# Kernel tuning notes

Measured on AMD Instinct MI355X. Metric: run time of the kernel, lower is better.

## Reference

```python
import jax, jax.numpy as jnp
import numpy as np

EPS = 1e-7


def _chamfer(p1, p2):
    # p1: (bs, N, 3), p2: (bs, M, 3)
    n1 = jnp.sum(p1 * p1, axis=-1)                    # (bs, N)
    n2 = jnp.sum(p2 * p2, axis=-1)                    # (bs, M)
    inner = jnp.einsum('bnd,bmd->bnm', p1, p2)        # (bs, N, M)
    d2 = n1[:, :, None] + n2[:, None, :] - 2.0 * inner
    d = jnp.sqrt(jnp.maximum(d2, 1e-12))              # L2 norm, as torch.norm(dim=3)
    # symmetric chamfer: sum of per-point nearest-neighbor distances, both ways
    cd = jnp.sum(jnp.min(d, axis=2)) + jnp.sum(jnp.min(d, axis=1))
    return cd


def setup_inputs() -> dict:
    key = jax.random.key(0)
    k1, k2, k3, k4, k5, k6, k7 = jax.random.split(key, 7)
    bs, K, N, M = 8, 1000, 4096, 4096
    return {
        'prob_pred': jax.random.uniform(k1, (bs, K), dtype=jnp.float32),
        'prob_target': jax.random.uniform(k2, (bs, K), dtype=jnp.float32),
        'x_diff_pred': jax.random.normal(k3, (bs, N, 3), dtype=jnp.float32),
        'x_diff_target': jax.random.normal(k4, (bs, M, 3), dtype=jnp.float32),
        'mu': jax.random.normal(k5, (K,), dtype=jnp.float32),
        'lower_bound': jax.random.uniform(k6, (K,), dtype=jnp.float32),
        'upper_bound': jax.random.uniform(k7, (K,), dtype=jnp.float32),
    }


def reference(prob_pred, prob_target, x_diff_pred, x_diff_target, mu, lower_bound, upper_bound):
    K = upper_bound.shape[0]
    # box-constraint term
    cr = jnp.abs(mu.reshape(lower_bound.shape)) - (lower_bound + upper_bound) / 2.0 + 1.0 / K
    CR = jnp.sum(jax.nn.relu(cr))
    # BCE with mean reduction (clamp like torch's internal log clamping)
    p = jnp.clip(prob_pred, EPS, 1.0 - EPS)
    BCE = -jnp.mean(prob_target * jnp.log(p) + (1.0 - prob_target) * jnp.log1p(-p))
    # chamfer distance
    CD = _chamfer(x_diff_pred, x_diff_target)
    return BCE + CD + CR
```

## Files before the change

### kernel.cpp

```cpp
#include <hip/hip_runtime.h>
#include <math.h>

#define EPSF 1e-7f
#define NP 4096

typedef __attribute__((ext_vector_type(8)))  short  short8;
typedef __attribute__((ext_vector_type(8)))  __bf16 bf16x8;
typedef __attribute__((ext_vector_type(16))) float  f32x16;

__device__ __forceinline__ unsigned short bf16_rn(float x) {
    unsigned int u = __float_as_uint(x);
    unsigned int r = u + 0x7FFFu + ((u >> 16) & 1u);
    return (unsigned short)(r >> 16);
}
__device__ __forceinline__ float bf16_to_f(unsigned short h) {
    return __uint_as_float(((unsigned int)h) << 16);
}

__device__ __forceinline__ void fold16(const f32x16& d, float& ra, float& rb) {
    ra = fminf(fminf(d[0],  d[1]),  ra);
    rb = fminf(fminf(d[2],  d[3]),  rb);
    ra = fminf(fminf(d[4],  d[5]),  ra);
    rb = fminf(fminf(d[6],  d[7]),  rb);
    ra = fminf(fminf(d[8],  d[9]),  ra);
    rb = fminf(fminf(d[10], d[11]), rb);
    ra = fminf(fminf(d[12], d[13]), ra);
    rb = fminf(fminf(d[14], d[15]), rb);
}

__device__ __forceinline__ bf16x8 make_qfrag(float x, float y, float z, int kg) {
    float m2x = -2.f * x, m2y = -2.f * y, m2z = -2.f * z;
    unsigned short xh = bf16_rn(m2x), yh = bf16_rn(m2y), zh = bf16_rn(m2z);
    unsigned short xl = bf16_rn(m2x - bf16_to_f(xh));
    unsigned short yl = bf16_rn(m2y - bf16_to_f(yh));
    unsigned short zl = bf16_rn(m2z - bf16_to_f(zh));
    short8 s;
    if (kg == 0)
        s = short8{(short)xh,(short)yh,(short)zh,(short)xl,(short)yl,(short)zl,(short)xh,(short)yh};
    else
        s = short8{(short)zh,(short)0x3F80,(short)0x3F80,0,0,0,0,0};
    return __builtin_bit_cast(bf16x8, s);
}

__global__ __launch_bounds__(256, 2) void chamfer_all(
    const float* __restrict__ pred, const float* __restrict__ targ,
    float* __restrict__ parts)
{
    const int tid  = threadIdx.x;
    const int lane = tid & 63, w = tid >> 6, kg = lane >> 5;
    const int strip = blockIdx.x;
    const int combo = blockIdx.y;
    const int dir = combo >> 3, b = combo & 7;

    __shared__ char  lds[65536];
    __shared__ float red[4];

    const float* Q = (dir ? targ : pred) + (size_t)b * NP * 3;
    const int q = strip * 128 + w * 32 + (lane & 31);
    const float qx = Q[q * 3], qy = Q[q * 3 + 1], qz = Q[q * 3 + 2];
    const bf16x8 frag = make_qfrag(qx, qy, qz, kg);
    const float n1 = fmaf(qx, qx, fmaf(qy, qy, qz * qz));

    const float* D = (dir ? pred : targ) + (size_t)b * NP * 3;

    float r0 = 3.4e38f, r1 = 3.4e38f;
    const f32x16 zero = {0.f};

    for (int half = 0; half < 2; ++half) {
#pragma unroll
        for (int i = 0; i < 8; ++i) {
            const int pl = tid + i * 256;
            const float* dp = D + (size_t)(half * 2048 + pl) * 3;
            float x = dp[0], y = dp[1], z = dp[2];
            float n2 = fmaf(x, x, fmaf(y, y, z * z));
            unsigned short xh = bf16_rn(x), yh = bf16_rn(y), zh = bf16_rn(z);
            unsigned short xl = bf16_rn(x - bf16_to_f(xh));
            unsigned short yl = bf16_rn(y - bf16_to_f(yh));
            unsigned short zl = bf16_rn(z - bf16_to_f(zh));
            unsigned short nh = bf16_rn(n2);
            unsigned short nl = bf16_rn(n2 - bf16_to_f(nh));
            short8 k0 = short8{(short)xh,(short)yh,(short)zh,
                               (short)xh,(short)yh,(short)zh,
                               (short)xl,(short)yl};
            short8 k1 = short8{(short)zl,(short)nh,(short)nl,0,0,0,0,0};
            char* base = lds + (pl >> 5) * 1024 + (pl & 31) * 16;
            *(short8*)base         = k0;
            *(short8*)(base + 512) = k1;
        }
        __syncthreads();

#pragma unroll 4
        for (int t = 0; t < 64; ++t) {
            bf16x8 af = *(const bf16x8*)(lds + t * 1024 + kg * 512 + (lane & 31) * 16);
            f32x16 d = __builtin_amdgcn_mfma_f32_32x32x16_bf16(af, frag, zero, 0, 0, 0);
            fold16(d, r0, r1);
        }
        __syncthreads();
    }

    float r = fminf(r0, r1);
    r = fminf(r, __shfl_xor(r, 32));
    float dist = sqrtf(fmaxf(r + n1, 1e-12f));
    for (int off = 16; off; off >>= 1) dist += __shfl_xor(dist, off);
    if (lane == 0) red[w] = dist;
    __syncthreads();
    if (tid == 0)
        parts[blockIdx.y * 32 + blockIdx.x] = red[0] + red[1] + red[2] + red[3];
}

__global__ __launch_bounds__(256) void finalize_kernel(
    const float* __restrict__ parts,
    const float* __restrict__ prob_pred, const float* __restrict__ prob_target,
    const float* __restrict__ mu, const float* __restrict__ lb,
    const float* __restrict__ ub,
    float* __restrict__ out, int nprob, int K)
{
    const int tid = threadIdx.x;

    float bce = 0.f;
    const float pmax = 1.0f - EPSF;
    for (int i = tid; i < nprob; i += 256) {
        float p = prob_pred[i];
        p = fminf(fmaxf(p, EPSF), pmax);
        float t = prob_target[i];
        bce += t * logf(p) + (1.0f - t) * log1pf(-p);
    }

    float cr = 0.f;
    const float invK = 1.0f / (float)K;
    for (int i = tid; i < K; i += 256) {
        float c = fabsf(mu[i]) - 0.5f * (lb[i] + ub[i]) + invK;
        cr += fmaxf(c, 0.f);
    }

    float v1 = parts[tid] + parts[tid + 256] + cr;
    float v2 = bce;
    for (int off = 32; off; off >>= 1) {
        v1 += __shfl_xor(v1, off);
        v2 += __shfl_xor(v2, off);
    }
    __shared__ float s1[4], s2[4];
    if ((tid & 63) == 0) { s1[tid >> 6] = v1; s2[tid >> 6] = v2; }
    __syncthreads();
    if (tid == 0) {
        float V1 = s1[0] + s1[1] + s1[2] + s1[3];
        float V2 = s2[0] + s2[1] + s2[2] + s2[3];
        out[0] = V1 - V2 / (float)nprob;
    }
}

extern "C" void kernel_launch(void* const* d_in, const int* in_sizes, int n_in,
                              void* d_out, int out_size, void* d_ws, size_t ws_size,
                              hipStream_t stream) {
    const float* prob_pred   = (const float*)d_in[0];
    const float* prob_target = (const float*)d_in[1];
    const float* x_pred      = (const float*)d_in[2];
    const float* x_target    = (const float*)d_in[3];
    const float* mu          = (const float*)d_in[4];
    const float* lb          = (const float*)d_in[5];
    const float* ub          = (const float*)d_in[6];
    float* out   = (float*)d_out;
    float* parts = (float*)d_ws;

    const int K     = in_sizes[4];
    const int nprob = in_sizes[0];

    dim3 grid(32, 16);
    chamfer_all<<<grid, 256, 0, stream>>>(x_pred, x_target, parts);
    finalize_kernel<<<1, 256, 0, stream>>>(parts, prob_pred, prob_target,
                                           mu, lb, ub, out, nprob, K);
}
```

Measured before the change: 29.70 us.

## Stage full reference panel once, split across 8 waves, two query tiles each

The chamfer kernel now loads and packs all 4096 reference points into a 128 KB LDS panel in one pass. Each 512-thread block handles 256 queries, with two query fragments per wave so each LDS A-fragment feeds two MFMAs. The two wave halves each scan half of the panel and merge their minima through LDS. The next fragment load is software-prefetched. The grid halves to 256 blocks, which cuts redundant reference loading and packing, but the large LDS footprint limits occupancy to one block per CU.

```diff
diff --git a/kernel.cpp b/kernel.cpp
--- a/kernel.cpp
+++ b/kernel.cpp
@@ -42,70 +42,91 @@
     return __builtin_bit_cast(bf16x8, s);
 }
 
-__global__ __launch_bounds__(256, 2) void chamfer_all(
+__global__ __launch_bounds__(512, 2) void chamfer_fused(
     const float* __restrict__ pred, const float* __restrict__ targ,
     float* __restrict__ parts)
 {
     const int tid  = threadIdx.x;
     const int lane = tid & 63, w = tid >> 6, kg = lane >> 5;
+    const int half = w >> 2;
     const int strip = blockIdx.x;
     const int combo = blockIdx.y;
     const int dir = combo >> 3, b = combo & 7;
 
-    __shared__ char  lds[65536];
-    __shared__ float red[4];
+    __shared__ char  panel[131072];
+    __shared__ float redbuf[512];
+    __shared__ float red4[4];
 
     const float* Q = (dir ? targ : pred) + (size_t)b * NP * 3;
-    const int q = strip * 128 + w * 32 + (lane & 31);
-    const float qx = Q[q * 3], qy = Q[q * 3 + 1], qz = Q[q * 3 + 2];
-    const bf16x8 frag = make_qfrag(qx, qy, qz, kg);
-    const float n1 = fmaf(qx, qx, fmaf(qy, qy, qz * qz));
+    const int qA = strip * 256 + (w & 3) * 64 + (lane & 31);
+    const int qB = qA + 32;
+    const float ax = Q[qA * 3], ay = Q[qA * 3 + 1], az = Q[qA * 3 + 2];
+    const float bx = Q[qB * 3], by = Q[qB * 3 + 1], bz = Q[qB * 3 + 2];
+    const bf16x8 fragA = make_qfrag(ax, ay, az, kg);
+    const bf16x8 fragB = make_qfrag(bx, by, bz, kg);
+    const float n1A = fmaf(ax, ax, fmaf(ay, ay, az * az));
+    const float n1B = fmaf(bx, bx, fmaf(by, by, bz * bz));
 
     const float* D = (dir ? pred : targ) + (size_t)b * NP * 3;
+#pragma unroll
+    for (int i = 0; i < 8; ++i) {
+        const int pt = i * 512 + tid;
+        const float* dp = D + (size_t)pt * 3;
+        float x = dp[0], y = dp[1], z = dp[2];
+        float n2 = fmaf(x, x, fmaf(y, y, z * z));
+        unsigned short xh = bf16_rn(x), yh = bf16_rn(y), zh = bf16_rn(z);
+        unsigned short xl = bf16_rn(x - bf16_to_f(xh));
+        unsigned short yl = bf16_rn(y - bf16_to_f(yh));
+        unsigned short zl = bf16_rn(z - bf16_to_f(zh));
+        unsigned short nh = bf16_rn(n2);
+        unsigned short nl = bf16_rn(n2 - bf16_to_f(nh));
+        short8 k0 = short8{(short)xh,(short)yh,(short)zh,
+                           (short)xh,(short)yh,(short)zh,
+                           (short)xl,(short)yl};
+        short8 k1 = short8{(short)zl,(short)nh,(short)nl,0,0,0,0,0};
+        char* base = panel + (pt >> 5) * 1024 + (pt & 31) * 16;
+        *(short8*)base         = k0;
+        *(short8*)(base + 512) = k1;
+    }
+    __syncthreads();
 
-    float r0 = 3.4e38f, r1 = 3.4e38f;
+    float rA0 = 3.4e38f, rA1 = 3.4e38f, rB0 = 3.4e38f, rB1 = 3.4e38f;
     const f32x16 zero = {0.f};
+    const char* abase = panel + (size_t)half * 65536 + kg * 512 + (lane & 31) * 16;
 
-    for (int half = 0; half < 2; ++half) {
-#pragma unroll
-        for (int i = 0; i < 8; ++i) {
-            const int pl = tid + i * 256;
-            const float* dp = D + (size_t)(half * 2048 + pl) * 3;
-            float x = dp[0], y = dp[1], z = dp[2];
-            float n2 = fmaf(x, x, fmaf(y, y, z * z));
-            unsigned short xh = bf16_rn(x), yh = bf16_rn(y), zh = bf16_rn(z);
-            unsigned short xl = bf16_rn(x - bf16_to_f(xh));
-            unsigned short yl = bf16_rn(y - bf16_to_f(yh));
-            unsigned short zl = bf16_rn(z - bf16_to_f(zh));
-            unsigned short nh = bf16_rn(n2);
-            unsigned short nl = bf16_rn(n2 - bf16_to_f(nh));
-            short8 k0 = short8{(short)xh,(short)yh,(short)zh,
-                               (short)xh,(short)yh,(short)zh,
-                               (short)xl,(short)yl};
-            short8 k1 = short8{(short)zl,(short)nh,(short)nl,0,0,0,0,0};
-            char* base = lds + (pl >> 5) * 1024 + (pl & 31) * 16;
-            *(short8*)base         = k0;
-            *(short8*)(base + 512) = k1;
-        }
-        __syncthreads();
-
+    bf16x8 af = *(const bf16x8*)(abase);
 #pragma unroll 4
-        for (int t = 0; t < 64; ++t) {
-            bf16x8 af = *(const bf16x8*)(lds + t * 1024 + kg * 512 + (lane & 31) * 16);
-            f32x16 d = __builtin_amdgcn_mfma_f32_32x32x16_bf16(af, frag, zero, 0, 0, 0);
-            fold16(d, r0, r1);
-        }
-        __syncthreads();
+    for (int t = 0; t < 63; ++t) {
+        bf16x8 afn = *(const bf16x8*)(abase + (t + 1) * 1024);
+        f32x16 d0 = __builtin_amdgcn_mfma_f32_32x32x16_bf16(af, fragA, zero, 0, 0, 0);
+        f32x16 d1 = __builtin_amdgcn_mfma_f32_32x32x16_bf16(af, fragB, zero, 0, 0, 0);
+        fold16(d0, rA0, rA1);
+        fold16(d1, rB0, rB1);
+        af = afn;
+    }
+    {
+        f32x16 d0 = __builtin_amdgcn_mfma_f32_32x32x16_bf16(af, fragA, zero, 0, 0, 0);
+        f32x16 d1 = __builtin_amdgcn_mfma_f32_32x32x16_bf16(af, fragB, zero, 0, 0, 0);
+        fold16(d0, rA0, rA1);
+        fold16(d1, rB0, rB1);
     }
 
-    float r = fminf(r0, r1);
-    r = fminf(r, __shfl_xor(r, 32));
-    float dist = sqrtf(fmaxf(r + n1, 1e-12f));
-    for (int off = 16; off; off >>= 1) dist += __shfl_xor(dist, off);
-    if (lane == 0) red[w] = dist;
+    float rA = fminf(rA0, rA1);  rA = fminf(rA, __shfl_xor(rA, 32));
+    float rB = fminf(rB0, rB1);  rB = fminf(rB, __shfl_xor(rB, 32));
+    float val = (lane < 32) ? (rA + n1A) : (rB + n1B);
+    __syncthreads();
+    redbuf[half * 256 + (w & 3) * 64 + lane] = val;
+    __syncthreads();
+
+    if (tid < 256) {
+        float m = fminf(redbuf[tid], redbuf[256 + tid]);
+        float dist = sqrtf(fmaxf(m, 1e-12f));
+        for (int off = 32; off; off >>= 1) dist += __shfl_xor(dist, off);
+        if ((tid & 63) == 0) red4[tid >> 6] = dist;
+    }
     __syncthreads();
     if (tid == 0)
-        parts[blockIdx.y * 32 + blockIdx.x] = red[0] + red[1] + red[2] + red[3];
+        parts[blockIdx.y * 16 + blockIdx.x] = red4[0] + red4[1] + red4[2] + red4[3];
 }
 
 __global__ __launch_bounds__(256) void finalize_kernel(
@@ -133,7 +154,7 @@
         cr += fmaxf(c, 0.f);
     }
 
-    float v1 = parts[tid] + parts[tid + 256] + cr;
+    float v1 = parts[tid] + cr;
     float v2 = bce;
     for (int off = 32; off; off >>= 1) {
         v1 += __shfl_xor(v1, off);
@@ -165,8 +186,8 @@
     const int K     = in_sizes[4];
     const int nprob = in_sizes[0];
 
-    dim3 grid(32, 16);
-    chamfer_all<<<grid, 256, 0, stream>>>(x_pred, x_target, parts);
+    dim3 grid(16, 16);
+    chamfer_fused<<<grid, 512, 0, stream>>>(x_pred, x_target, parts);
     finalize_kernel<<<1, 256, 0, stream>>>(parts, prob_pred, prob_target,
                                            mu, lb, ub, out, nprob, K);
 }
```

Result: faster. 28.93 us (-2.6%).
